# Kernel optimization log

Measured on AMD Instinct MI355X. Metric: run time of the kernel, lower is better.

Reference implementation:

```python
import jax, jax.numpy as jnp
import numpy as np
import math

B, C_IN, C_QK, H, W, NH = 1, 256, 128, 96, 96, 8
SCALE = math.sqrt(C_QK / NH)  # sqrt(planes/num_head) = 4.0
TEMP = 1.0


def conv1x1(x, w, b=None):
    # x: [B, Cin, H, W], w: [Cout, Cin] -> [B, Cout, H, W]
    y = jnp.einsum('bchw,oc->bohw', x, w)
    if b is not None:
        y = y + b[None, :, None, None]
    return y


def maxpool2x2(x):
    return jax.lax.reduce_window(x, -jnp.inf, jax.lax.max,
                                 (1, 1, 2, 2), (1, 1, 2, 2), 'VALID')


def setup_inputs() -> dict:
    key = jax.random.key(0)
    ks = jax.random.split(key, 5)
    x = jax.random.normal(ks[0], (B, C_IN, H, W), dtype=jnp.float32)
    # conv weights: init.normal_(w, 0, 0.01), zero bias; conv_value has no bias
    w_q = jax.random.normal(ks[1], (C_QK, C_IN), dtype=jnp.float32) * 0.01
    b_q = jnp.zeros((C_QK,), dtype=jnp.float32)
    w_k = jax.random.normal(ks[2], (C_QK, C_IN), dtype=jnp.float32) * 0.01
    b_k = jnp.zeros((C_QK,), dtype=jnp.float32)
    w_v = jax.random.normal(ks[3], (C_IN, C_IN), dtype=jnp.float32) * 0.01
    return {'x': x, 'w_q': w_q, 'b_q': b_q, 'w_k': w_k, 'b_k': b_k, 'w_v': w_v}


def reference(x, w_q, b_q, w_k, b_k, w_v):
    residual = x
    input_x = maxpool2x2(x)                       # [B, Cin, H/2, W/2]
    Hd, Wd = H // 2, W // 2
    Nq, Nk = H * W, Hd * Wd

    q = conv1x1(x, w_q, b_q)                      # [B, Cqk, H, W]
    k = conv1x1(input_x, w_k, b_k)                # [B, Cqk, Hd, Wd]
    v = conv1x1(input_x, w_v)                     # [B, Cin, Hd, Wd]

    dq = C_QK // NH
    dv = C_IN // NH
    q = q.reshape(B * NH, dq, Nq)
    k = k.reshape(B * NH, dq, Nk)
    v = v.reshape(B * NH, dv, Nk)

    # dot distance: scaled by sqrt(planes/num_head) and temp (nowd empty)
    sim = jnp.einsum('bdq,bdk->bqk', q, k) / (SCALE * TEMP)
    attn = jax.nn.softmax(sim, axis=2)            # softmax over keys

    # out = value @ attn^T  -> [B*NH, dv, Nq]
    out = jnp.einsum('bdk,bqk->bdq', v, attn)
    out = out.reshape(B, C_IN, H, W)
    return out + residual
```

## Files before the change

### kernel.cpp

```cpp
#include <hip/hip_runtime.h>
#include <hip/hip_bf16.h>
#include <math.h>

#define C_IN   256
#define C_QK   128
#define NH     8
#define H_     96
#define W_     96
#define NQ     (H_*W_)
#define HD     48
#define WD     48
#define NK     (HD*WD)
#define DQ     16
#define DV     32
#define NQC    (NQ/32)
#define NKC    (NK/32)
#define KQRT   (NKC/4)
#define KSTEPS (C_IN/16)
#define QS     0.3606737602222409f

typedef __attribute__((ext_vector_type(8)))  short short8v;
typedef __attribute__((ext_vector_type(16))) float f32x16;
typedef __attribute__((ext_vector_type(2)))  int   v2i;

union B8u { uint u[4]; short8v v; };

static __device__ inline ushort bf16r(float f) {
    __hip_bfloat16 h = __float2bfloat16(f);
    return *reinterpret_cast<ushort*>(&h);
}
static __device__ inline uint cvtpk(float lo, float hi) {
    uint r;
    asm("v_cvt_pk_bf16_f32 %0, %1, %2" : "=v"(r) : "v"(lo), "v"(hi));
    return r;
}
static __device__ inline void lswap(uint a, uint b, uint& x, uint& y, int hi) {
#if __has_builtin(__builtin_amdgcn_permlane32_swap)
    v2i r = __builtin_amdgcn_permlane32_swap((int)a, (int)b, false, false);
    x = (uint)r.x;
    y = (uint)r.y;
#else
    uint bx = (uint)__shfl_xor((int)b, 32);
    uint ax = (uint)__shfl_xor((int)a, 32);
    x = hi ? bx : a;
    y = hi ? b : ax;
#endif
}
static __device__ inline float fexp2(float v) {
#if __has_builtin(__builtin_amdgcn_exp2f)
    return __builtin_amdgcn_exp2f(v);
#else
    return __expf(v * 0.6931471805599453f);
#endif
}

#define U_XB   (NQC*KSTEPS*64)
#define U_XPB  (NKC*KSTEPS*64)
#define U_WQ   (4*KSTEPS*64)
#define U_WK   (4*KSTEPS*64)
#define U_WV   (8*KSTEPS*64)
#define U_FRAG (U_XB+U_XPB+U_WQ+U_WK+U_WV)
#define U_TOT  (U_FRAG + 128)

__global__ __launch_bounds__(256) void prep_kernel(
    const float* __restrict__ x,  const float* __restrict__ wq, const float* __restrict__ bq,
    const float* __restrict__ wk, const float* __restrict__ wv,
    ushort* __restrict__ xbP, ushort* __restrict__ xpbP,
    ushort* __restrict__ wqP, ushort* __restrict__ wkP, ushort* __restrict__ wvP,
    float* __restrict__ bqs)
{
    int t = blockIdx.x * 256 + threadIdx.x;
    if (t >= U_TOT) return;
    if (t >= U_FRAG) { int i = t - U_FRAG; bqs[i] = bq[i] * QS; return; }

    union { ushort s[8]; uint4 v; } ou;
    int u = t;
    if (u < U_XB) {
        int l = u & 63, rest = u >> 6;
        int ks = rest & 15, nc = rest >> 4;
        int n  = nc * 32 + (l & 31);
        int k0 = ks * 16 + 8 * (l >> 5);
        #pragma unroll
        for (int j = 0; j < 8; ++j) ou.s[j] = bf16r(x[(size_t)(k0 + j) * NQ + n]);
        *(uint4*)&xbP[(size_t)u * 8] = ou.v;
        return;
    }
    u -= U_XB;
    if (u < U_XPB) {
        int l = u & 63, rest = u >> 6;
        int ks = rest & 15, nc = rest >> 4;
        int np = nc * 32 + (l & 31);
        int k0 = ks * 16 + 8 * (l >> 5);
        int py = np / WD, px = np - py * WD;
        const float* base = x + (2 * py) * W_ + 2 * px;
        #pragma unroll
        for (int j = 0; j < 8; ++j) {
            const float* p = base + (size_t)(k0 + j) * NQ;
            ou.s[j] = bf16r(fmaxf(fmaxf(p[0], p[1]), fmaxf(p[W_], p[W_ + 1])));
        }
        *(uint4*)&xpbP[(size_t)u * 8] = ou.v;
        return;
    }
    u -= U_XPB;
    if (u < U_WQ) {
        int l = u & 63, ks = (u >> 6) & 15, mb = u >> 10;
        int m = mb * 32 + (l & 31), k0 = ks * 16 + 8 * (l >> 5);
        #pragma unroll
        for (int j = 0; j < 8; ++j) ou.s[j] = bf16r(wq[m * C_IN + k0 + j] * QS);
        *(uint4*)&wqP[(size_t)u * 8] = ou.v;
        return;
    }
    u -= U_WQ;
    if (u < U_WK) {
        int l = u & 63, ks = (u >> 6) & 15, mb = u >> 10;
        int m = mb * 32 + (l & 31), k0 = ks * 16 + 8 * (l >> 5);
        #pragma unroll
        for (int j = 0; j < 8; ++j) ou.s[j] = bf16r(wk[m * C_IN + k0 + j]);
        *(uint4*)&wkP[(size_t)u * 8] = ou.v;
        return;
    }
    u -= U_WK;
    {
        int l = u & 63, ks = (u >> 6) & 15, cb = u >> 10;
        int c = cb * 32 + (l & 31), k0 = ks * 16 + 8 * (l >> 5);
        #pragma unroll
        for (int j = 0; j < 8; ++j) ou.s[j] = bf16r(wv[c * C_IN + k0 + j]);
        *(uint4*)&wvP[(size_t)u * 8] = ou.v;
    }
}

static __device__ inline f32x16 mfma_loop(const ushort* __restrict__ A,
                                          const ushort* __restrict__ B) {
    f32x16 acc;
    #pragma unroll
    for (int r = 0; r < 16; ++r) acc[r] = 0.0f;
    #pragma unroll
    for (int s = 0; s < KSTEPS; ++s) {
        short8v a = *(const short8v*)(A + (size_t)s * 512);
        short8v b = *(const short8v*)(B + (size_t)s * 512);
        acc = __builtin_amdgcn_mfma_f32_32x32x16_bf16(a, b, acc, 0, 0, 0);
    }
    return acc;
}
static __device__ inline void xform(const f32x16& acc, int hi, short8v& F1, short8v& F2) {
    uint a0 = cvtpk(acc[0],  acc[1]),  a1 = cvtpk(acc[2],  acc[3]);
    uint b0 = cvtpk(acc[4],  acc[5]),  b1 = cvtpk(acc[6],  acc[7]);
    uint a2 = cvtpk(acc[8],  acc[9]),  a3 = cvtpk(acc[10], acc[11]);
    uint b2 = cvtpk(acc[12], acc[13]), b3 = cvtpk(acc[14], acc[15]);
    B8u f1, f2;
    lswap(a0, b0, f1.u[0], f1.u[2], hi);
    lswap(a1, b1, f1.u[1], f1.u[3], hi);
    lswap(a2, b2, f2.u[0], f2.u[2], hi);
    lswap(a3, b3, f2.u[1], f2.u[3], hi);
    F1 = f1.v; F2 = f2.v;
}

#define T_Q 1152
#define T_K (T_Q + 288)
#define T_ALL (T_K + 576)

__global__ __launch_bounds__(256) void gemm_fused(
    const ushort* __restrict__ xbP, const ushort* __restrict__ xpbP,
    const ushort* __restrict__ wqP, const ushort* __restrict__ wkP,
    const ushort* __restrict__ wvP,
    const float* __restrict__ bqs, const float* __restrict__ bk,
    ushort* __restrict__ qpack, ushort* __restrict__ kpack, ushort* __restrict__ vpack)
{
    int lane = threadIdx.x & 63, wvi = threadIdx.x >> 6;
    int hi = lane >> 5;
    int t = blockIdx.x * 4 + wvi;
    if (t >= T_ALL) return;

    if (t < T_Q) {
        int mb = t / NQC, nc = t - mb * NQC;
        const ushort* A = wqP + ((size_t)(mb * KSTEPS) * 64 + lane) * 8;
        const ushort* B = xbP + ((size_t)(nc * KSTEPS) * 64 + lane) * 8;
        f32x16 acc = mfma_loop(A, B);
        #pragma unroll
        for (int r = 0; r < 16; ++r)
            acc[r] += bqs[mb * 32 + (r & 3) + 8 * (r >> 2) + 4 * hi];
        short8v F1, F2;
        xform(acc, hi, F1, F2);
        *(short8v*)&qpack[((size_t)((2 * mb)     * NQC + nc) * 64 + lane) * 8] = F1;
        *(short8v*)&qpack[((size_t)((2 * mb + 1) * NQC + nc) * 64 + lane) * 8] = F2;
    } else if (t < T_K) {
        int t2 = t - T_Q;
        int mb = t2 / NKC, nc = t2 - mb * NKC;
        const ushort* A = wkP  + ((size_t)(mb * KSTEPS) * 64 + lane) * 8;
        const ushort* B = xpbP + ((size_t)(nc * KSTEPS) * 64 + lane) * 8;
        f32x16 acc = mfma_loop(A, B);
        #pragma unroll
        for (int r = 0; r < 16; ++r)
            acc[r] += bk[mb * 32 + (r & 3) + 8 * (r >> 2) + 4 * hi];
        short8v F1, F2;
        xform(acc, hi, F1, F2);
        *(short8v*)&kpack[((size_t)((2 * mb)     * NKC + nc) * 64 + lane) * 8] = F1;
        *(short8v*)&kpack[((size_t)((2 * mb + 1) * NKC + nc) * 64 + lane) * 8] = F2;
    } else {
        int t3 = t - T_K;
        int cb = t3 / NKC, kc = t3 - cb * NKC;
        const ushort* A = xpbP + ((size_t)(kc * KSTEPS) * 64 + lane) * 8;
        const ushort* B = wvP  + ((size_t)(cb * KSTEPS) * 64 + lane) * 8;
        f32x16 acc = mfma_loop(A, B);
        short8v F1, F2;
        xform(acc, hi, F1, F2);
        *(short8v*)&vpack[((size_t)((cb * NKC + kc) * 2 + 0) * 64 + lane) * 8] = F1;
        *(short8v*)&vpack[((size_t)((cb * NKC + kc) * 2 + 1) * 64 + lane) * 8] = F2;
    }
}

#define CSTR 17

__global__ __launch_bounds__(256) void attn_kernel(const ushort* __restrict__ qpack,
                                                   const ushort* __restrict__ kpack,
                                                   const ushort* __restrict__ vpack,
                                                   const float* __restrict__ x,
                                                   float* __restrict__ out) {
    __shared__ float part[4][64][CSTR];
    const int h = blockIdx.y, qc = blockIdx.x;
    const int tid = threadIdx.x, lane = tid & 63;
    const int kh = tid >> 6;
    const int q31 = lane & 31, hi = lane >> 5;

    short8v qf = *(const short8v*)&qpack[((size_t)(h * NQC + qc) * 64 + lane) * 8];

    const ushort* kp = kpack + ((size_t)(h * NKC + kh * KQRT) * 64 + lane) * 8;
    const ushort* vp = vpack + ((size_t)(h * NKC + kh * KQRT) * 2 * 64 + lane) * 8;

    short8v kf = *(const short8v*)kp;
    short8v v0 = *(const short8v*)vp;

    f32x16 o, zc;
    #pragma unroll
    for (int r = 0; r < 16; ++r) { o[r] = 0.0f; zc[r] = 0.0f; }
    float rs = 0.0f;

    for (int c = 0; c < KQRT; ++c) {
        short8v kcur = kf, v0c = v0;
        short8v v1c = *(const short8v*)(vp + (size_t)c * 1024 + 512);
        int cn = (c == KQRT - 1) ? 0 : (c + 1);
        kf = *(const short8v*)(kp + (size_t)cn * 512);
        v0 = *(const short8v*)(vp + (size_t)cn * 1024);

        f32x16 s = __builtin_amdgcn_mfma_f32_32x32x16_bf16(kcur, qf, zc, 0, 0, 0);
        {
            float e0 = fexp2(s[0]), e1 = fexp2(s[1]), e2 = fexp2(s[2]), e3 = fexp2(s[3]);
            float e4 = fexp2(s[4]), e5 = fexp2(s[5]), e6 = fexp2(s[6]), e7 = fexp2(s[7]);
            rs += ((e0 + e1) + (e2 + e3)) + ((e4 + e5) + (e6 + e7));
            uint a0 = cvtpk(e0, e1), a1 = cvtpk(e2, e3);
            uint b0 = cvtpk(e4, e5), b1 = cvtpk(e6, e7);
            B8u B1;
            lswap(a0, b0, B1.u[0], B1.u[2], hi);
            lswap(a1, b1, B1.u[1], B1.u[3], hi);
            o = __builtin_amdgcn_mfma_f32_32x32x16_bf16(v0c, B1.v, o, 0, 0, 0);
        }
        {
            float e0 = fexp2(s[8]),  e1 = fexp2(s[9]),  e2 = fexp2(s[10]), e3 = fexp2(s[11]);
            float e4 = fexp2(s[12]), e5 = fexp2(s[13]), e6 = fexp2(s[14]), e7 = fexp2(s[15]);
            rs += ((e0 + e1) + (e2 + e3)) + ((e4 + e5) + (e6 + e7));
            uint a0 = cvtpk(e0, e1), a1 = cvtpk(e2, e3);
            uint b0 = cvtpk(e4, e5), b1 = cvtpk(e6, e7);
            B8u B2;
            lswap(a0, b0, B2.u[0], B2.u[2], hi);
            lswap(a1, b1, B2.u[1], B2.u[3], hi);
            o = __builtin_amdgcn_mfma_f32_32x32x16_bf16(v1c, B2.v, o, 0, 0, 0);
        }
    }

    rs += __shfl_xor(rs, 32);

    {
        float* pw = &part[kh][lane][0];
        #pragma unroll
        for (int r = 0; r < 16; ++r) pw[r] = o[r];
        pw[16] = rs;
    }
    __syncthreads();

    float rsAll = part[0][lane][16] + part[1][lane][16]
                + part[2][lane][16] + part[3][lane][16];
    float inv = 1.0f / rsAll;
    int q = qc * 32 + q31;
    #pragma unroll
    for (int i = 0; i < 4; ++i) {
        int r = 4 * kh + i;
        float val = part[0][lane][r] + part[1][lane][r]
                  + part[2][lane][r] + part[3][lane][r];
        int dv = i + 8 * kh + 4 * hi;
        size_t i0 = (size_t)(h * DV + dv) * NQ + q;
        out[i0] = val * inv + x[i0];
    }
}

extern "C" void kernel_launch(void* const* d_in, const int* in_sizes, int n_in,
                              void* d_out, int out_size, void* d_ws, size_t ws_size,
                              hipStream_t stream) {
    const float* x  = (const float*)d_in[0];
    const float* wq = (const float*)d_in[1];
    const float* bq = (const float*)d_in[2];
    const float* wk = (const float*)d_in[3];
    const float* bk = (const float*)d_in[4];
    const float* wv = (const float*)d_in[5];
    float* out = (float*)d_out;

    ushort* p = (ushort*)d_ws;
    ushort* xbP   = p;  p += (size_t)U_XB  * 8;
    ushort* xpbP  = p;  p += (size_t)U_XPB * 8;
    ushort* wqP   = p;  p += (size_t)U_WQ  * 8;
    ushort* wkP   = p;  p += (size_t)U_WK  * 8;
    ushort* wvP   = p;  p += (size_t)U_WV  * 8;
    ushort* qpack = p;  p += (size_t)NH * NQC * 64 * 8;
    ushort* kpack = p;  p += (size_t)NH * NKC * 64 * 8;
    ushort* vpack = p;  p += (size_t)NH * NKC * 2 * 64 * 8;
    float*  bqs   = (float*)p;

    prep_kernel<<<(U_TOT + 255) / 256, 256, 0, stream>>>(x, wq, bq, wk, wv,
                                                         xbP, xpbP, wqP, wkP, wvP, bqs);
    gemm_fused<<<(T_ALL + 3) / 4, 256, 0, stream>>>(xbP, xpbP, wqP, wkP, wvP,
                                                    bqs, bk, qpack, kpack, vpack);
    attn_kernel<<<dim3(NQC, NH), 256, 0, stream>>>(qpack, kpack, vpack, x, out);
}
```

Measured before the change: 114.6 us.

## Fuse bf16 packing prep into projection GEMM and restructure attention loop prefetch

Removes the separate prep kernel: the projection GEMM kernel now converts x (and max-pooled x) tiles to bf16 directly into shared memory and converts fp32 weights on the fly per k-step. This drops one launch and the write/read round trip of the packed intermediate buffers, at the cost of redundant weight conversion per block. Q scaling now applies after the bias add instead of being baked into pre-scaled weights. The attention loop is restructured into a prefetch-next pipeline with split row-sum accumulators and unroll 2.

After: 111.9 us. 2.3% less time.

```diff
diff --git a/kernel.cpp b/kernel.cpp
--- a/kernel.cpp
+++ b/kernel.cpp
@@ -25,10 +25,6 @@
 
 union B8u { uint u[4]; short8v v; };
 
-static __device__ inline ushort bf16r(float f) {
-    __hip_bfloat16 h = __float2bfloat16(f);
-    return *reinterpret_cast<ushort*>(&h);
-}
 static __device__ inline uint cvtpk(float lo, float hi) {
     uint r;
     asm("v_cvt_pk_bf16_f32 %0, %1, %2" : "=v"(r) : "v"(lo), "v"(hi));
@@ -54,162 +50,177 @@
 #endif
 }
 
-#define U_XB   (NQC*KSTEPS*64)
-#define U_XPB  (NKC*KSTEPS*64)
-#define U_WQ   (4*KSTEPS*64)
-#define U_WK   (4*KSTEPS*64)
-#define U_WV   (8*KSTEPS*64)
-#define U_FRAG (U_XB+U_XPB+U_WQ+U_WK+U_WV)
-#define U_TOT  (U_FRAG + 128)
-
-__global__ __launch_bounds__(256) void prep_kernel(
-    const float* __restrict__ x,  const float* __restrict__ wq, const float* __restrict__ bq,
-    const float* __restrict__ wk, const float* __restrict__ wv,
-    ushort* __restrict__ xbP, ushort* __restrict__ xpbP,
-    ushort* __restrict__ wqP, ushort* __restrict__ wkP, ushort* __restrict__ wvP,
-    float* __restrict__ bqs)
+#define GQ_B 288
+#define GK_B (GQ_B + 72)
+#define G_ALL (GK_B + 144)
+
+__global__ __launch_bounds__(256) void gemm_all(
+    const float* __restrict__ x,
+    const float* __restrict__ wq, const float* __restrict__ bq,
+    const float* __restrict__ wk, const float* __restrict__ bk_,
+    const float* __restrict__ wv,
+    ushort* __restrict__ qpack, ushort* __restrict__ kpack, ushort* __restrict__ vpack)
 {
-    int t = blockIdx.x * 256 + threadIdx.x;
-    if (t >= U_TOT) return;
-    if (t >= U_FRAG) { int i = t - U_FRAG; bqs[i] = bq[i] * QS; return; }
-
-    union { ushort s[8]; uint4 v; } ou;
-    int u = t;
-    if (u < U_XB) {
-        int l = u & 63, rest = u >> 6;
-        int ks = rest & 15, nc = rest >> 4;
-        int n  = nc * 32 + (l & 31);
-        int k0 = ks * 16 + 8 * (l >> 5);
-        #pragma unroll
-        for (int j = 0; j < 8; ++j) ou.s[j] = bf16r(x[(size_t)(k0 + j) * NQ + n]);
-        *(uint4*)&xbP[(size_t)u * 8] = ou.v;
-        return;
-    }
-    u -= U_XB;
-    if (u < U_XPB) {
-        int l = u & 63, rest = u >> 6;
-        int ks = rest & 15, nc = rest >> 4;
-        int np = nc * 32 + (l & 31);
-        int k0 = ks * 16 + 8 * (l >> 5);
-        int py = np / WD, px = np - py * WD;
-        const float* base = x + (2 * py) * W_ + 2 * px;
-        #pragma unroll
-        for (int j = 0; j < 8; ++j) {
-            const float* p = base + (size_t)(k0 + j) * NQ;
-            ou.s[j] = bf16r(fmaxf(fmaxf(p[0], p[1]), fmaxf(p[W_], p[W_ + 1])));
+    __shared__ ushort Bf[KSTEPS][64][8];
+    const int tid = threadIdx.x, lane = tid & 63, wvi = tid >> 6;
+    const int hi = lane >> 5;
+    const int bid = blockIdx.x;
+
+    {
+        int c = tid & 31;
+        int ko0 = (tid >> 5) * 4;
+        if (bid < GQ_B) {
+            int col = bid * 32 + c;
+            #pragma unroll
+            for (int u = 0; u < 4; ++u) {
+                int ko = ko0 + u;
+                const float* xp_ = x + (size_t)(8 * ko) * NQ + col;
+                float f[8];
+                #pragma unroll
+                for (int j = 0; j < 8; ++j) f[j] = xp_[(size_t)j * NQ];
+                uint4 w;
+                w.x = cvtpk(f[0], f[1]); w.y = cvtpk(f[2], f[3]);
+                w.z = cvtpk(f[4], f[5]); w.w = cvtpk(f[6], f[7]);
+                *(uint4*)&Bf[ko >> 1][32 * (ko & 1) + c][0] = w;
+            }
+        } else {
+            int kc = (bid < GK_B) ? (bid - GQ_B) : ((bid - GK_B) >> 1);
+            int np = kc * 32 + c;
+            int py = np / WD, px = np - py * WD;
+            const float* base = x + (2 * py) * W_ + 2 * px;
+            #pragma unroll
+            for (int u = 0; u < 4; ++u) {
+                int ko = ko0 + u;
+                const float* xp_ = base + (size_t)(8 * ko) * NQ;
+                float f[8];
+                #pragma unroll
+                for (int j = 0; j < 8; ++j) {
+                    const float* p = xp_ + (size_t)j * NQ;
+                    f[j] = fmaxf(fmaxf(p[0], p[1]), fmaxf(p[W_], p[W_ + 1]));
+                }
+                uint4 w;
+                w.x = cvtpk(f[0], f[1]); w.y = cvtpk(f[2], f[3]);
+                w.z = cvtpk(f[4], f[5]); w.w = cvtpk(f[6], f[7]);
+                *(uint4*)&Bf[ko >> 1][32 * (ko & 1) + c][0] = w;
+            }
         }
-        *(uint4*)&xpbP[(size_t)u * 8] = ou.v;
-        return;
-    }
-    u -= U_XPB;
-    if (u < U_WQ) {
-        int l = u & 63, ks = (u >> 6) & 15, mb = u >> 10;
-        int m = mb * 32 + (l & 31), k0 = ks * 16 + 8 * (l >> 5);
-        #pragma unroll
-        for (int j = 0; j < 8; ++j) ou.s[j] = bf16r(wq[m * C_IN + k0 + j] * QS);
-        *(uint4*)&wqP[(size_t)u * 8] = ou.v;
-        return;
-    }
-    u -= U_WQ;
-    if (u < U_WK) {
-        int l = u & 63, ks = (u >> 6) & 15, mb = u >> 10;
-        int m = mb * 32 + (l & 31), k0 = ks * 16 + 8 * (l >> 5);
-        #pragma unroll
-        for (int j = 0; j < 8; ++j) ou.s[j] = bf16r(wk[m * C_IN + k0 + j]);
-        *(uint4*)&wkP[(size_t)u * 8] = ou.v;
-        return;
-    }
-    u -= U_WK;
-    {
-        int l = u & 63, ks = (u >> 6) & 15, cb = u >> 10;
-        int c = cb * 32 + (l & 31), k0 = ks * 16 + 8 * (l >> 5);
-        #pragma unroll
-        for (int j = 0; j < 8; ++j) ou.s[j] = bf16r(wv[c * C_IN + k0 + j]);
-        *(uint4*)&wvP[(size_t)u * 8] = ou.v;
-    }
-}
-
-static __device__ inline f32x16 mfma_loop(const ushort* __restrict__ A,
-                                          const ushort* __restrict__ B) {
+    }
+    __syncthreads();
+
     f32x16 acc;
     #pragma unroll
     for (int r = 0; r < 16; ++r) acc[r] = 0.0f;
+
+    const float* Wsrc;
+    if (bid < GQ_B)      Wsrc = wq + (size_t)(wvi * 32 + (lane & 31)) * C_IN + 8 * hi;
+    else if (bid < GK_B) Wsrc = wk + (size_t)(wvi * 32 + (lane & 31)) * C_IN + 8 * hi;
+    else {
+        int cb = ((bid - GK_B) & 1) * 4 + wvi;
+        Wsrc = wv + (size_t)(cb * 32 + (lane & 31)) * C_IN + 8 * hi;
+    }
+
     #pragma unroll
     for (int s = 0; s < KSTEPS; ++s) {
-        short8v a = *(const short8v*)(A + (size_t)s * 512);
-        short8v b = *(const short8v*)(B + (size_t)s * 512);
-        acc = __builtin_amdgcn_mfma_f32_32x32x16_bf16(a, b, acc, 0, 0, 0);
-    }
-    return acc;
-}
-static __device__ inline void xform(const f32x16& acc, int hi, short8v& F1, short8v& F2) {
-    uint a0 = cvtpk(acc[0],  acc[1]),  a1 = cvtpk(acc[2],  acc[3]);
-    uint b0 = cvtpk(acc[4],  acc[5]),  b1 = cvtpk(acc[6],  acc[7]);
-    uint a2 = cvtpk(acc[8],  acc[9]),  a3 = cvtpk(acc[10], acc[11]);
-    uint b2 = cvtpk(acc[12], acc[13]), b3 = cvtpk(acc[14], acc[15]);
-    B8u f1, f2;
-    lswap(a0, b0, f1.u[0], f1.u[2], hi);
-    lswap(a1, b1, f1.u[1], f1.u[3], hi);
-    lswap(a2, b2, f2.u[0], f2.u[2], hi);
-    lswap(a3, b3, f2.u[1], f2.u[3], hi);
-    F1 = f1.v; F2 = f2.v;
-}
-
-#define T_Q 1152
-#define T_K (T_Q + 288)
-#define T_ALL (T_K + 576)
-
-__global__ __launch_bounds__(256) void gemm_fused(
-    const ushort* __restrict__ xbP, const ushort* __restrict__ xpbP,
-    const ushort* __restrict__ wqP, const ushort* __restrict__ wkP,
-    const ushort* __restrict__ wvP,
-    const float* __restrict__ bqs, const float* __restrict__ bk,
-    ushort* __restrict__ qpack, ushort* __restrict__ kpack, ushort* __restrict__ vpack)
-{
-    int lane = threadIdx.x & 63, wvi = threadIdx.x >> 6;
-    int hi = lane >> 5;
-    int t = blockIdx.x * 4 + wvi;
-    if (t >= T_ALL) return;
-
-    if (t < T_Q) {
-        int mb = t / NQC, nc = t - mb * NQC;
-        const ushort* A = wqP + ((size_t)(mb * KSTEPS) * 64 + lane) * 8;
-        const ushort* B = xbP + ((size_t)(nc * KSTEPS) * 64 + lane) * 8;
-        f32x16 acc = mfma_loop(A, B);
+        float4 wa = *(const float4*)(Wsrc + 16 * s);
+        float4 wb = *(const float4*)(Wsrc + 16 * s + 4);
+        B8u af;
+        af.u[0] = cvtpk(wa.x, wa.y); af.u[1] = cvtpk(wa.z, wa.w);
+        af.u[2] = cvtpk(wb.x, wb.y); af.u[3] = cvtpk(wb.z, wb.w);
+        short8v b = *(const short8v*)&Bf[s][lane][0];
+        if (bid < GK_B)
+            acc = __builtin_amdgcn_mfma_f32_32x32x16_bf16(af.v, b, acc, 0, 0, 0);
+        else
+            acc = __builtin_amdgcn_mfma_f32_32x32x16_bf16(b, af.v, acc, 0, 0, 0);
+    }
+
+    short8v F1, F2;
+    if (bid < GQ_B) {
+        int nc = bid, mb = wvi;
         #pragma unroll
         for (int r = 0; r < 16; ++r)
-            acc[r] += bqs[mb * 32 + (r & 3) + 8 * (r >> 2) + 4 * hi];
-        short8v F1, F2;
-        xform(acc, hi, F1, F2);
+            acc[r] = (acc[r] + bq[mb * 32 + (r & 3) + 8 * (r >> 2) + 4 * hi]) * QS;
+        {
+            uint a0 = cvtpk(acc[0],  acc[1]),  a1 = cvtpk(acc[2],  acc[3]);
+            uint b0 = cvtpk(acc[4],  acc[5]),  b1 = cvtpk(acc[6],  acc[7]);
+            uint a2 = cvtpk(acc[8],  acc[9]),  a3 = cvtpk(acc[10], acc[11]);
+            uint b2 = cvtpk(acc[12], acc[13]), b3 = cvtpk(acc[14], acc[15]);
+            B8u f1, f2;
+            lswap(a0, b0, f1.u[0], f1.u[2], hi);
+            lswap(a1, b1, f1.u[1], f1.u[3], hi);
+            lswap(a2, b2, f2.u[0], f2.u[2], hi);
+            lswap(a3, b3, f2.u[1], f2.u[3], hi);
+            F1 = f1.v; F2 = f2.v;
+        }
         *(short8v*)&qpack[((size_t)((2 * mb)     * NQC + nc) * 64 + lane) * 8] = F1;
         *(short8v*)&qpack[((size_t)((2 * mb + 1) * NQC + nc) * 64 + lane) * 8] = F2;
-    } else if (t < T_K) {
-        int t2 = t - T_Q;
-        int mb = t2 / NKC, nc = t2 - mb * NKC;
-        const ushort* A = wkP  + ((size_t)(mb * KSTEPS) * 64 + lane) * 8;
-        const ushort* B = xpbP + ((size_t)(nc * KSTEPS) * 64 + lane) * 8;
-        f32x16 acc = mfma_loop(A, B);
+    } else if (bid < GK_B) {
+        int nc = bid - GQ_B, mb = wvi;
         #pragma unroll
         for (int r = 0; r < 16; ++r)
-            acc[r] += bk[mb * 32 + (r & 3) + 8 * (r >> 2) + 4 * hi];
-        short8v F1, F2;
-        xform(acc, hi, F1, F2);
+            acc[r] += bk_[mb * 32 + (r & 3) + 8 * (r >> 2) + 4 * hi];
+        {
+            uint a0 = cvtpk(acc[0],  acc[1]),  a1 = cvtpk(acc[2],  acc[3]);
+            uint b0 = cvtpk(acc[4],  acc[5]),  b1 = cvtpk(acc[6],  acc[7]);
+            uint a2 = cvtpk(acc[8],  acc[9]),  a3 = cvtpk(acc[10], acc[11]);
+            uint b2 = cvtpk(acc[12], acc[13]), b3 = cvtpk(acc[14], acc[15]);
+            B8u f1, f2;
+            lswap(a0, b0, f1.u[0], f1.u[2], hi);
+            lswap(a1, b1, f1.u[1], f1.u[3], hi);
+            lswap(a2, b2, f2.u[0], f2.u[2], hi);
+            lswap(a3, b3, f2.u[1], f2.u[3], hi);
+            F1 = f1.v; F2 = f2.v;
+        }
         *(short8v*)&kpack[((size_t)((2 * mb)     * NKC + nc) * 64 + lane) * 8] = F1;
         *(short8v*)&kpack[((size_t)((2 * mb + 1) * NKC + nc) * 64 + lane) * 8] = F2;
     } else {
-        int t3 = t - T_K;
-        int cb = t3 / NKC, kc = t3 - cb * NKC;
-        const ushort* A = xpbP + ((size_t)(kc * KSTEPS) * 64 + lane) * 8;
-        const ushort* B = wvP  + ((size_t)(cb * KSTEPS) * 64 + lane) * 8;
-        f32x16 acc = mfma_loop(A, B);
-        short8v F1, F2;
-        xform(acc, hi, F1, F2);
+        int vb = bid - GK_B;
+        int kc = vb >> 1, cb = (vb & 1) * 4 + wvi;
+        {
+            uint a0 = cvtpk(acc[0],  acc[1]),  a1 = cvtpk(acc[2],  acc[3]);
+            uint b0 = cvtpk(acc[4],  acc[5]),  b1 = cvtpk(acc[6],  acc[7]);
+            uint a2 = cvtpk(acc[8],  acc[9]),  a3 = cvtpk(acc[10], acc[11]);
+            uint b2 = cvtpk(acc[12], acc[13]), b3 = cvtpk(acc[14], acc[15]);
+            B8u f1, f2;
+            lswap(a0, b0, f1.u[0], f1.u[2], hi);
+            lswap(a1, b1, f1.u[1], f1.u[3], hi);
+            lswap(a2, b2, f2.u[0], f2.u[2], hi);
+            lswap(a3, b3, f2.u[1], f2.u[3], hi);
+            F1 = f1.v; F2 = f2.v;
+        }
         *(short8v*)&vpack[((size_t)((cb * NKC + kc) * 2 + 0) * 64 + lane) * 8] = F1;
         *(short8v*)&vpack[((size_t)((cb * NKC + kc) * 2 + 1) * 64 + lane) * 8] = F2;
     }
 }
 
 #define CSTR 17
+
+static __device__ inline void attn_step(short8v kc_, short8v qf, short8v v0c, short8v v1c,
+                                        f32x16& o, float& rsA, float& rsB,
+                                        const f32x16& zc, int hi) {
+    f32x16 s = __builtin_amdgcn_mfma_f32_32x32x16_bf16(kc_, qf, zc, 0, 0, 0);
+    {
+        float e0 = fexp2(s[0]), e1 = fexp2(s[1]), e2 = fexp2(s[2]), e3 = fexp2(s[3]);
+        float e4 = fexp2(s[4]), e5 = fexp2(s[5]), e6 = fexp2(s[6]), e7 = fexp2(s[7]);
+        rsA += ((e0 + e1) + (e2 + e3)) + ((e4 + e5) + (e6 + e7));
+        uint a0 = cvtpk(e0, e1), a1 = cvtpk(e2, e3);
+        uint b0 = cvtpk(e4, e5), b1 = cvtpk(e6, e7);
+        B8u B1;
+        lswap(a0, b0, B1.u[0], B1.u[2], hi);
+        lswap(a1, b1, B1.u[1], B1.u[3], hi);
+        o = __builtin_amdgcn_mfma_f32_32x32x16_bf16(v0c, B1.v, o, 0, 0, 0);
+    }
+    {
+        float e0 = fexp2(s[8]),  e1 = fexp2(s[9]),  e2 = fexp2(s[10]), e3 = fexp2(s[11]);
+        float e4 = fexp2(s[12]), e5 = fexp2(s[13]), e6 = fexp2(s[14]), e7 = fexp2(s[15]);
+        rsB += ((e0 + e1) + (e2 + e3)) + ((e4 + e5) + (e6 + e7));
+        uint a0 = cvtpk(e0, e1), a1 = cvtpk(e2, e3);
+        uint b0 = cvtpk(e4, e5), b1 = cvtpk(e6, e7);
+        B8u B2;
+        lswap(a0, b0, B2.u[0], B2.u[2], hi);
+        lswap(a1, b1, B2.u[1], B2.u[3], hi);
+        o = __builtin_amdgcn_mfma_f32_32x32x16_bf16(v1c, B2.v, o, 0, 0, 0);
+    }
+}
 
 __global__ __launch_bounds__(256) void attn_kernel(const ushort* __restrict__ qpack,
                                                    const ushort* __restrict__ kpack,
@@ -224,49 +235,30 @@
 
     short8v qf = *(const short8v*)&qpack[((size_t)(h * NQC + qc) * 64 + lane) * 8];
 
-    const ushort* kp = kpack + ((size_t)(h * NKC + kh * KQRT) * 64 + lane) * 8;
-    const ushort* vp = vpack + ((size_t)(h * NKC + kh * KQRT) * 2 * 64 + lane) * 8;
-
-    short8v kf = *(const short8v*)kp;
-    short8v v0 = *(const short8v*)vp;
+    const char* kp = (const char*)(kpack + ((size_t)(h * NKC + kh * KQRT) * 64 + lane) * 8);
+    const char* vp = (const char*)(vpack + ((size_t)(h * NKC + kh * KQRT) * 2 * 64 + lane) * 8);
+
+    short8v kf  = *(const short8v*)kp;
+    short8v v0f = *(const short8v*)vp;
+    short8v v1f = *(const short8v*)(vp + 1024);
 
     f32x16 o, zc;
     #pragma unroll
     for (int r = 0; r < 16; ++r) { o[r] = 0.0f; zc[r] = 0.0f; }
-    float rs = 0.0f;
-
-    for (int c = 0; c < KQRT; ++c) {
-        short8v kcur = kf, v0c = v0;
-        short8v v1c = *(const short8v*)(vp + (size_t)c * 1024 + 512);
-        int cn = (c == KQRT - 1) ? 0 : (c + 1);
-        kf = *(const short8v*)(kp + (size_t)cn * 512);
-        v0 = *(const short8v*)(vp + (size_t)cn * 1024);
-
-        f32x16 s = __builtin_amdgcn_mfma_f32_32x32x16_bf16(kcur, qf, zc, 0, 0, 0);
-        {
-            float e0 = fexp2(s[0]), e1 = fexp2(s[1]), e2 = fexp2(s[2]), e3 = fexp2(s[3]);
-            float e4 = fexp2(s[4]), e5 = fexp2(s[5]), e6 = fexp2(s[6]), e7 = fexp2(s[7]);
-            rs += ((e0 + e1) + (e2 + e3)) + ((e4 + e5) + (e6 + e7));
-            uint a0 = cvtpk(e0, e1), a1 = cvtpk(e2, e3);
-            uint b0 = cvtpk(e4, e5), b1 = cvtpk(e6, e7);
-            B8u B1;
-            lswap(a0, b0, B1.u[0], B1.u[2], hi);
-            lswap(a1, b1, B1.u[1], B1.u[3], hi);
-            o = __builtin_amdgcn_mfma_f32_32x32x16_bf16(v0c, B1.v, o, 0, 0, 0);
-        }
-        {
-            float e0 = fexp2(s[8]),  e1 = fexp2(s[9]),  e2 = fexp2(s[10]), e3 = fexp2(s[11]);
-            float e4 = fexp2(s[12]), e5 = fexp2(s[13]), e6 = fexp2(s[14]), e7 = fexp2(s[15]);
-            rs += ((e0 + e1) + (e2 + e3)) + ((e4 + e5) + (e6 + e7));
-            uint a0 = cvtpk(e0, e1), a1 = cvtpk(e2, e3);
-            uint b0 = cvtpk(e4, e5), b1 = cvtpk(e6, e7);
-            B8u B2;
-            lswap(a0, b0, B2.u[0], B2.u[2], hi);
-            lswap(a1, b1, B2.u[1], B2.u[3], hi);
-            o = __builtin_amdgcn_mfma_f32_32x32x16_bf16(v1c, B2.v, o, 0, 0, 0);
-        }
-    }
-
+    float rsA = 0.0f, rsB = 0.0f;
+
+    #pragma unroll 2
+    for (int c = 0; c < KQRT - 1; ++c) {
+        kp += 1024; vp += 2048;
+        short8v kn  = *(const short8v*)kp;
+        short8v v0n = *(const short8v*)vp;
+        short8v v1n = *(const short8v*)(vp + 1024);
+        attn_step(kf, qf, v0f, v1f, o, rsA, rsB, zc, hi);
+        kf = kn; v0f = v0n; v1f = v1n;
+    }
+    attn_step(kf, qf, v0f, v1f, o, rsA, rsB, zc, hi);
+
+    float rs = rsA + rsB;
     rs += __shfl_xor(rs, 32);
 
     {
@@ -304,19 +296,10 @@
     float* out = (float*)d_out;
 
     ushort* p = (ushort*)d_ws;
-    ushort* xbP   = p;  p += (size_t)U_XB  * 8;
-    ushort* xpbP  = p;  p += (size_t)U_XPB * 8;
-    ushort* wqP   = p;  p += (size_t)U_WQ  * 8;
-    ushort* wkP   = p;  p += (size_t)U_WK  * 8;
-    ushort* wvP   = p;  p += (size_t)U_WV  * 8;
     ushort* qpack = p;  p += (size_t)NH * NQC * 64 * 8;
     ushort* kpack = p;  p += (size_t)NH * NKC * 64 * 8;
     ushort* vpack = p;  p += (size_t)NH * NKC * 2 * 64 * 8;
-    float*  bqs   = (float*)p;
-
-    prep_kernel<<<(U_TOT + 255) / 256, 256, 0, stream>>>(x, wq, bq, wk, wv,
-                                                         xbP, xpbP, wqP, wkP, wvP, bqs);
-    gemm_fused<<<(T_ALL + 3) / 4, 256, 0, stream>>>(xbP, xpbP, wqP, wkP, wvP,
-                                                    bqs, bk, qpack, kpack, vpack);
+
+    gemm_all<<<G_ALL, 256, 0, stream>>>(x, wq, bq, wk, bk, wv, qpack, kpack, vpack);
     attn_kernel<<<dim3(NQC, NH), 256, 0, stream>>>(qpack, kpack, vpack, x, out);
 }
```
